# Performance work log

Measured on AMD Instinct MI355X. Metric: run time of the kernel, lower is better.

The kernel has to match this reference:

```python
import jax, jax.numpy as jnp
import numpy as np

D_IN, D_DICT, K, N = 768, 16384, 32, 8192


def setup_inputs() -> dict:
    key = jax.random.key(0)
    k1, k2, k3, k4, k5 = jax.random.split(key, 5)
    s_in = 1.0 / np.sqrt(D_IN)
    s_dict = 1.0 / np.sqrt(D_DICT)
    return {
        "x": jax.random.normal(k1, (N, D_IN), dtype=jnp.float32),
        # torch Linear: weight [out, in], bias [out]
        "W_enc": jax.random.uniform(k2, (D_DICT, D_IN), jnp.float32, -s_in, s_in),
        "b_enc": jax.random.uniform(k3, (D_DICT,), jnp.float32, -s_in, s_in),
        "W_dec": jax.random.uniform(k4, (D_IN, D_DICT), jnp.float32, -s_dict, s_dict),
        "b_dec": jax.random.uniform(k5, (D_IN,), jnp.float32, -s_dict, s_dict),
    }


def reference(x, W_enc, b_enc, W_dec, b_dec):
    # encode: z = x @ W_enc^T + b_enc  -> [N, d_dict]
    z = jnp.einsum("nd,kd->nk", x, W_enc) + b_enc
    # top-k mask along last dim (scatter 1.0 at top-k indices)
    _, idx = jax.lax.top_k(z, K)                      # idx: [N, K]
    rows = jnp.arange(z.shape[0])[:, None]            # [N, 1]
    mask = jnp.zeros_like(z).at[rows, idx].set(1.0)
    z_sparse = z * mask
    # decode: x_hat = z_sparse @ W_dec^T + b_dec -> [N, d_in]
    x_hat = jnp.einsum("nk,dk->nd", z_sparse, W_dec) + b_dec
    return (x_hat, z_sparse)
```

## Files before the change

### kernel.cpp

```cpp
#include <hip/hip_runtime.h>
#include <stdint.h>

#define D_IN   768
#define D_DICT 16384
#define NROWS  8192
#define TOPK   32
#define CAND_TARGET 40
#define CAND_MAX    80

typedef __attribute__((ext_vector_type(4))) float  f32x4;
typedef __attribute__((ext_vector_type(8))) short  s16x8;
typedef __attribute__((ext_vector_type(4))) unsigned short u16x4;

static __device__ __forceinline__ unsigned short f2bf(float f) {
    unsigned int u = __float_as_uint(f);
    unsigned int r = (u + 0x7FFFu + ((u >> 16) & 1u)) >> 16;
    return (unsigned short)r;
}

static __device__ __forceinline__ void gload_lds16(const void* g, void* l) {
    __builtin_amdgcn_global_load_lds(
        (const __attribute__((address_space(1))) unsigned int*)g,
        (__attribute__((address_space(3))) unsigned int*)l, 16, 0, 0);
}

__global__ __launch_bounds__(256) void cast_bf16(const float4* __restrict__ in,
                                                 u16x4* __restrict__ out, int n4) {
    int idx = blockIdx.x * 256 + threadIdx.x;
    if (idx >= n4) return;
    float4 v = in[idx];
    u16x4 o;
    o.x = f2bf(v.x); o.y = f2bf(v.y); o.z = f2bf(v.z); o.w = f2bf(v.w);
    out[idx] = o;
}

__global__ void transpose_wdec(const float* __restrict__ in, float* __restrict__ out) {
    __shared__ float t[32][33];
    int bx = blockIdx.x;
    int by = blockIdx.y;
    int tx = threadIdx.x;
    int ty = threadIdx.y;
#pragma unroll
    for (int i = 0; i < 4; ++i)
        t[ty + i * 8][tx] = in[(size_t)(by * 32 + ty + i * 8) * D_DICT + bx * 32 + tx];
    __syncthreads();
#pragma unroll
    for (int i = 0; i < 4; ++i)
        out[(size_t)(bx * 32 + ty + i * 8) * D_IN + by * 32 + tx] = t[tx][ty + i * 8];
}

__global__ __launch_bounds__(256) void gemm_enc(const unsigned short* __restrict__ Xb,
                                                const unsigned short* __restrict__ Wb,
                                                const float* __restrict__ bEnc,
                                                float* __restrict__ zbase) {
    __shared__ unsigned short As[128 * 64];
    __shared__ unsigned short Bs[128 * 64];
    const int tid    = threadIdx.x;
    const int waveId = tid >> 6;
    const int lane   = tid & 63;
    const int rowBase = blockIdx.y * 128;
    const int colBase = blockIdx.x * 128;
    const int wm = waveId >> 1, wn = waveId & 1;

    f32x4 acc[4][4] = {};

    const int m0 = wm * 64 + (lane & 15);
    const int n0 = wn * 64 + (lane & 15);
    const int kq = (lane >> 4) * 8;

    for (int k0 = 0; k0 < D_IN; k0 += 64) {
#pragma unroll
        for (int i = 0; i < 4; ++i) {
            int slot = i * 256 + tid;
            int r = slot >> 3, cc = (slot & 7) * 8;
            const unsigned short* ga = Xb + (size_t)(rowBase + r) * D_IN + k0 + cc;
            const unsigned short* gb = Wb + (size_t)(colBase + r) * D_IN + k0 + cc;
            unsigned short* la = As + (size_t)(i * 256 + waveId * 64) * 8;
            unsigned short* lb = Bs + (size_t)(i * 256 + waveId * 64) * 8;
            gload_lds16(ga, la);
            gload_lds16(gb, lb);
        }
        __syncthreads();
#pragma unroll
        for (int kk = 0; kk < 64; kk += 32) {
            s16x8 a[4], b[4];
#pragma unroll
            for (int t = 0; t < 4; ++t) {
                a[t] = *(const s16x8*)(As + (m0 + t * 16) * 64 + kk + kq);
                b[t] = *(const s16x8*)(Bs + (n0 + t * 16) * 64 + kk + kq);
            }
#pragma unroll
            for (int mi = 0; mi < 4; ++mi)
#pragma unroll
                for (int ni = 0; ni < 4; ++ni)
                    acc[mi][ni] = __builtin_amdgcn_mfma_f32_16x16x32_bf16(
                        a[mi], b[ni], acc[mi][ni], 0, 0, 0);
        }
        __syncthreads();
    }

    const int col0 = colBase + wn * 64 + (lane & 15);
    const int rq   = (lane >> 4) * 4;
#pragma unroll
    for (int ni = 0; ni < 4; ++ni) {
        int gc = col0 + ni * 16;
        float bias = bEnc[gc];
#pragma unroll
        for (int mi = 0; mi < 4; ++mi) {
            int gr0 = rowBase + wm * 64 + mi * 16 + rq;
#pragma unroll
            for (int rg = 0; rg < 4; ++rg) {
                float v = acc[mi][ni][rg] + bias;
                ((unsigned short*)(zbase + (size_t)(gr0 + rg) * D_DICT))[gc] = f2bf(v);
            }
        }
    }
}

__global__ __launch_bounds__(256) void rowpass(const float* __restrict__ x,
                                               const float* __restrict__ wEnc,
                                               const float* __restrict__ bEnc,
                                               const float* __restrict__ bDec,
                                               const float* __restrict__ wDecT,
                                               float* __restrict__ xhat,
                                               float* __restrict__ zsp) {
    const int row = blockIdx.x;
    const int tid = threadIdx.x;

    __shared__ unsigned short zrow[D_DICT];
    __shared__ int   hist[256];
    __shared__ float xs[D_IN];
    __shared__ int   cidx[CAND_MAX];
    __shared__ float zc[CAND_MAX];
    __shared__ int   selk[TOPK];
    __shared__ float selv[TOPK];
    __shared__ int   sh_nstrict, sh_ntie, sh_nsel, sh_cutHi, sh_cumAbove, sh_cut;

    hist[tid] = 0;
    if (tid == 0) { sh_nstrict = 0; sh_ntie = 0; sh_nsel = 0; }
    __syncthreads();

    const unsigned short* zr = (const unsigned short*)(zsp + (size_t)row * D_DICT);
#pragma unroll 2
    for (int i = 0; i < 8; ++i) {
        uint4 raw = ((const uint4*)zr)[i * 256 + tid];
        unsigned int w[4] = {raw.x, raw.y, raw.z, raw.w};
        int base = (i * 256 + tid) * 8;
#pragma unroll
        for (int q = 0; q < 4; ++q) {
#pragma unroll
            for (int h = 0; h < 2; ++h) {
                unsigned short u = (unsigned short)((w[q] >> (16 * h)) & 0xFFFFu);
                u = (u & 0x8000u) ? (unsigned short)(~u) : (unsigned short)(u | 0x8000u);
                zrow[base + q * 2 + h] = u;
                atomicAdd(&hist[u >> 8], 1);
            }
        }
    }
    for (int j = tid; j < D_IN; j += 256) xs[j] = x[(size_t)row * D_IN + j];
    __syncthreads();

    {
        float4 z4 = make_float4(0.f, 0.f, 0.f, 0.f);
        float4* zd = (float4*)(zsp + (size_t)row * D_DICT);
#pragma unroll 4
        for (int i = 0; i < 16; ++i) zd[i * 256 + tid] = z4;
    }

    if (tid == 0) {
        int cum = 0, b = 255;
        for (; b >= 0; --b) {
            int c = cum + hist[b];
            if (c >= CAND_TARGET) break;
            cum = c;
        }
        sh_cutHi = b; sh_cumAbove = cum;
    }
    __syncthreads();
    const int cutHi = sh_cutHi;
    hist[tid] = 0;
    __syncthreads();
    for (int i = 0; i < 64; ++i) {
        unsigned short u = zrow[i * 256 + tid];
        if ((u >> 8) == cutHi) atomicAdd(&hist[u & 255], 1);
    }
    __syncthreads();
    if (tid == 0) {
        int cum = sh_cumAbove, b = 255;
        for (; b >= 0; --b) {
            int c = cum + hist[b];
            if (c >= CAND_TARGET) break;
            cum = c;
        }
        sh_cut = (cutHi << 8) | b;
    }
    __syncthreads();
    const unsigned short cut = (unsigned short)sh_cut;

    for (int i = 0; i < 64; ++i) {
        int idx = i * 256 + tid;
        unsigned short u = zrow[idx];
        if (u > cut) {
            int p = atomicAdd(&sh_nstrict, 1);
            cidx[p] = idx;
        } else if (u == cut) {
            int t = atomicAdd(&sh_ntie, 1);
            if (t < CAND_TARGET) cidx[CAND_MAX - 1 - t] = idx;
        }
    }
    __syncthreads();
    const int nstrict = sh_nstrict;
    const int nt = min(sh_ntie, CAND_TARGET);
    int tmpv = 0;
    if (tid < nt) tmpv = cidx[CAND_MAX - 1 - tid];
    __syncthreads();
    if (tid < nt) cidx[nstrict + tid] = tmpv;
    __syncthreads();
    const int nc = nstrict + nt;

    const int wave = tid >> 6, lane = tid & 63;
    for (int c = wave; c < nc; c += 4) {
        int k = cidx[c];
        const float* w = wEnc + (size_t)k * D_IN;
        double acc = 0.0;
#pragma unroll
        for (int i = 0; i < D_IN / 64; ++i) {
            int j = i * 64 + lane;
            acc += (double)xs[j] * (double)w[j];
        }
#pragma unroll
        for (int off = 32; off > 0; off >>= 1) acc += __shfl_xor(acc, off, 64);
        if (lane == 0) zc[c] = (float)(acc + (double)bEnc[k]);
    }
    __syncthreads();

    if (tid < nc) {
        float v = zc[tid];
        int   k = cidx[tid];
        int r = 0;
        for (int j = 0; j < nc; ++j) {
            float vj = zc[j];
            if (vj > v || (vj == v && cidx[j] < k)) ++r;
        }
        if (r < TOPK) {
            int s = atomicAdd(&sh_nsel, 1);
            selk[s] = k; selv[s] = v;
            zsp[(size_t)row * D_DICT + k] = v;
        }
    }
    __syncthreads();

    for (int d = tid; d < D_IN; d += 256) {
        float acc = bDec[d];
#pragma unroll
        for (int j = 0; j < TOPK; ++j)
            acc += selv[j] * wDecT[(size_t)selk[j] * D_IN + d];
        xhat[(size_t)row * D_IN + d] = acc;
    }
}

extern "C" void kernel_launch(void* const* d_in, const int* in_sizes, int n_in,
                              void* d_out, int out_size, void* d_ws, size_t ws_size,
                              hipStream_t stream) {
    const float* x    = (const float*)d_in[0];
    const float* wEnc = (const float*)d_in[1];
    const float* bEnc = (const float*)d_in[2];
    const float* wDec = (const float*)d_in[3];
    const float* bDec = (const float*)d_in[4];

    float* xhat = (float*)d_out;
    float* zsp  = (float*)d_out + (size_t)NROWS * D_IN;

    char* ws = (char*)d_ws;
    unsigned short* Xb  = (unsigned short*)ws;
    unsigned short* Wb  = (unsigned short*)(ws + (size_t)NROWS * D_IN * 2);
    float*          WdT = (float*)(ws + (size_t)NROWS * D_IN * 2
                                      + (size_t)D_DICT * D_IN * 2);

    {
        int n4 = NROWS * D_IN / 4;
        cast_bf16<<<(n4 + 255) / 256, 256, 0, stream>>>((const float4*)x, (u16x4*)Xb, n4);
    }
    {
        int n4 = D_DICT * D_IN / 4;
        cast_bf16<<<(n4 + 255) / 256, 256, 0, stream>>>((const float4*)wEnc, (u16x4*)Wb, n4);
    }
    transpose_wdec<<<dim3(D_DICT / 32, D_IN / 32), dim3(32, 8), 0, stream>>>(wDec, WdT);
    gemm_enc<<<dim3(D_DICT / 128, NROWS / 128), 256, 0, stream>>>(Xb, Wb, bEnc, zsp);
    rowpass<<<NROWS, 256, 0, stream>>>(x, wEnc, bEnc, bDec, WdT, xhat, zsp);
}
```

Baseline: 1.397 ms.

## Restructure top-k selection into register-resident histogram pass and separate decode kernel

The encoder GEMM now writes the order-preserving mapped bf16 scores into a densely packed buffer that aliases the z_sparse output. A new selection kernel keeps each row's scores in registers instead of staging them in LDS. It builds per-wave histograms, first over a floored range with a fallback to the full range, and finds the threshold bins with wave prefix scans and ballots rather than a serial single-thread loop. Candidate rescoring now uses four threads per candidate instead of a whole wave. Zeroing and scattering z_sparse and the decode move to a separate kernel, which is needed because the packed scores overlap the output; this costs an extra launch and a small index/value round trip through the workspace.

After: 1.352 ms. -3.2%, faster.

```diff
diff --git a/kernel.cpp b/kernel.cpp
--- a/kernel.cpp
+++ b/kernel.cpp
@@ -16,6 +16,9 @@
     unsigned int u = __float_as_uint(f);
     unsigned int r = (u + 0x7FFFu + ((u >> 16) & 1u)) >> 16;
     return (unsigned short)r;
+}
+static __device__ __forceinline__ unsigned short bfmap(unsigned short u) {
+    return (u & 0x8000u) ? (unsigned short)(~u) : (unsigned short)(u | 0x8000u);
 }
 
 static __device__ __forceinline__ void gload_lds16(const void* g, void* l) {
@@ -36,10 +39,8 @@
 
 __global__ void transpose_wdec(const float* __restrict__ in, float* __restrict__ out) {
     __shared__ float t[32][33];
-    int bx = blockIdx.x;
-    int by = blockIdx.y;
-    int tx = threadIdx.x;
-    int ty = threadIdx.y;
+    int bx = blockIdx.x, by = blockIdx.y;
+    int tx = threadIdx.x, ty = threadIdx.y;
 #pragma unroll
     for (int i = 0; i < 4; ++i)
         t[ty + i * 8][tx] = in[(size_t)(by * 32 + ty + i * 8) * D_DICT + bx * 32 + tx];
@@ -52,7 +53,7 @@
 __global__ __launch_bounds__(256) void gemm_enc(const unsigned short* __restrict__ Xb,
                                                 const unsigned short* __restrict__ Wb,
                                                 const float* __restrict__ bEnc,
-                                                float* __restrict__ zbase) {
+                                                unsigned short* __restrict__ zhat) {
     __shared__ unsigned short As[128 * 64];
     __shared__ unsigned short Bs[128 * 64];
     const int tid    = threadIdx.x;
@@ -111,102 +112,153 @@
 #pragma unroll
             for (int rg = 0; rg < 4; ++rg) {
                 float v = acc[mi][ni][rg] + bias;
-                ((unsigned short*)(zbase + (size_t)(gr0 + rg) * D_DICT))[gc] = f2bf(v);
-            }
-        }
-    }
-}
-
-__global__ __launch_bounds__(256) void rowpass(const float* __restrict__ x,
-                                               const float* __restrict__ wEnc,
-                                               const float* __restrict__ bEnc,
-                                               const float* __restrict__ bDec,
-                                               const float* __restrict__ wDecT,
-                                               float* __restrict__ xhat,
-                                               float* __restrict__ zsp) {
+                zhat[(size_t)(gr0 + rg) * D_DICT + gc] = bfmap(f2bf(v));
+            }
+        }
+    }
+}
+
+__global__ __launch_bounds__(256) void sel_topk(const unsigned short* __restrict__ zhat,
+                                                const float* __restrict__ x,
+                                                const float* __restrict__ wEnc,
+                                                const float* __restrict__ bEnc,
+                                                int* __restrict__ SelK,
+                                                float* __restrict__ SelV) {
     const int row = blockIdx.x;
     const int tid = threadIdx.x;
-
-    __shared__ unsigned short zrow[D_DICT];
-    __shared__ int   hist[256];
+    const int waveId = tid >> 6;
+
+    __shared__ int   histc[4][256];
     __shared__ float xs[D_IN];
     __shared__ int   cidx[CAND_MAX];
     __shared__ float zc[CAND_MAX];
     __shared__ int   selk[TOPK];
     __shared__ float selv[TOPK];
-    __shared__ int   sh_nstrict, sh_ntie, sh_nsel, sh_cutHi, sh_cumAbove, sh_cut;
-
-    hist[tid] = 0;
+    __shared__ int   sh_bin, sh_cum, sh_bin2;
+    __shared__ int   sh_nstrict, sh_ntie, sh_nsel;
+
+    uint4 r[8];
+    const uint4* zr4 = (const uint4*)(zhat + (size_t)row * D_DICT);
+#pragma unroll
+    for (int i = 0; i < 8; ++i) r[i] = zr4[i * 256 + tid];
+    for (int j = tid; j < D_IN; j += 256) xs[j] = x[(size_t)row * D_IN + j];
     if (tid == 0) { sh_nstrict = 0; sh_ntie = 0; sh_nsel = 0; }
-    __syncthreads();
-
-    const unsigned short* zr = (const unsigned short*)(zsp + (size_t)row * D_DICT);
-#pragma unroll 2
+
+    unsigned int floorU = 0xBE80u;
+    int shift1 = 6;
+    const int T = CAND_TARGET;
+
+    for (int att = 0; att < 2; ++att) {
+        for (int b = tid; b < 1024; b += 256) ((int*)histc)[b] = 0;
+        if (tid == 0) sh_bin = -1;
+        __syncthreads();
+#pragma unroll
+        for (int i = 0; i < 8; ++i) {
+            unsigned int w[4] = {r[i].x, r[i].y, r[i].z, r[i].w};
+#pragma unroll
+            for (int q = 0; q < 4; ++q)
+#pragma unroll
+                for (int h = 0; h < 2; ++h) {
+                    unsigned int u = (w[q] >> (16 * h)) & 0xFFFFu;
+                    if (u >= floorU) {
+                        int bin = (int)((u - floorU) >> shift1);
+                        if (bin > 255) bin = 255;
+                        atomicAdd(&histc[waveId][bin], 1);
+                    }
+                }
+        }
+        __syncthreads();
+        if (tid < 256) histc[0][tid] += histc[1][tid] + histc[2][tid] + histc[3][tid];
+        __syncthreads();
+        if (tid < 64) {
+            int l = tid;
+            int b0 = 255 - l * 4;
+            int s0 = histc[0][b0], s1 = histc[0][b0 - 1],
+                s2 = histc[0][b0 - 2], s3 = histc[0][b0 - 3];
+            int local = s0 + s1 + s2 + s3;
+            int pref = local;
+#pragma unroll
+            for (int off = 1; off < 64; off <<= 1) {
+                int n = __shfl_up(pref, off, 64);
+                if (l >= off) pref += n;
+            }
+            unsigned long long m = __ballot(pref >= T);
+            if (m) {
+                int first = (int)__ffsll(m) - 1;
+                if (l == first) {
+                    int cum = pref - local;
+                    int b, c;
+                    if      (cum + s0 >= T)           { b = b0;     c = cum; }
+                    else if (cum + s0 + s1 >= T)      { b = b0 - 1; c = cum + s0; }
+                    else if (cum + s0 + s1 + s2 >= T) { b = b0 - 2; c = cum + s0 + s1; }
+                    else                              { b = b0 - 3; c = cum + s0 + s1 + s2; }
+                    sh_bin = b; sh_cum = c;
+                }
+            }
+        }
+        __syncthreads();
+        if (sh_bin >= 0) break;
+        floorU = 0u; shift1 = 8;
+    }
+    const int b1 = sh_bin;
+    const int cumAbove = sh_cum;
+    const int s2 = shift1 - 6;
+
+    for (int b = tid; b < 1024; b += 256) ((int*)histc)[b] = 0;
+    __syncthreads();
+#pragma unroll
     for (int i = 0; i < 8; ++i) {
-        uint4 raw = ((const uint4*)zr)[i * 256 + tid];
-        unsigned int w[4] = {raw.x, raw.y, raw.z, raw.w};
-        int base = (i * 256 + tid) * 8;
-#pragma unroll
-        for (int q = 0; q < 4; ++q) {
+        unsigned int w[4] = {r[i].x, r[i].y, r[i].z, r[i].w};
+#pragma unroll
+        for (int q = 0; q < 4; ++q)
 #pragma unroll
             for (int h = 0; h < 2; ++h) {
-                unsigned short u = (unsigned short)((w[q] >> (16 * h)) & 0xFFFFu);
-                u = (u & 0x8000u) ? (unsigned short)(~u) : (unsigned short)(u | 0x8000u);
-                zrow[base + q * 2 + h] = u;
-                atomicAdd(&hist[u >> 8], 1);
-            }
-        }
-    }
-    for (int j = tid; j < D_IN; j += 256) xs[j] = x[(size_t)row * D_IN + j];
-    __syncthreads();
-
-    {
-        float4 z4 = make_float4(0.f, 0.f, 0.f, 0.f);
-        float4* zd = (float4*)(zsp + (size_t)row * D_DICT);
-#pragma unroll 4
-        for (int i = 0; i < 16; ++i) zd[i * 256 + tid] = z4;
-    }
-
-    if (tid == 0) {
-        int cum = 0, b = 255;
-        for (; b >= 0; --b) {
-            int c = cum + hist[b];
-            if (c >= CAND_TARGET) break;
-            cum = c;
-        }
-        sh_cutHi = b; sh_cumAbove = cum;
-    }
-    __syncthreads();
-    const int cutHi = sh_cutHi;
-    hist[tid] = 0;
-    __syncthreads();
-    for (int i = 0; i < 64; ++i) {
-        unsigned short u = zrow[i * 256 + tid];
-        if ((u >> 8) == cutHi) atomicAdd(&hist[u & 255], 1);
-    }
-    __syncthreads();
-    if (tid == 0) {
-        int cum = sh_cumAbove, b = 255;
-        for (; b >= 0; --b) {
-            int c = cum + hist[b];
-            if (c >= CAND_TARGET) break;
-            cum = c;
-        }
-        sh_cut = (cutHi << 8) | b;
-    }
-    __syncthreads();
-    const unsigned short cut = (unsigned short)sh_cut;
-
-    for (int i = 0; i < 64; ++i) {
-        int idx = i * 256 + tid;
-        unsigned short u = zrow[idx];
-        if (u > cut) {
-            int p = atomicAdd(&sh_nstrict, 1);
-            cidx[p] = idx;
-        } else if (u == cut) {
-            int t = atomicAdd(&sh_ntie, 1);
-            if (t < CAND_TARGET) cidx[CAND_MAX - 1 - t] = idx;
-        }
+                unsigned int u = (w[q] >> (16 * h)) & 0xFFFFu;
+                if (u >= floorU) {
+                    int bin = (int)((u - floorU) >> shift1);
+                    if (bin > 255) bin = 255;
+                    if (bin == b1) {
+                        int bin2 = (int)(((u - floorU) >> s2) & 63u);
+                        atomicAdd(&histc[waveId][bin2], 1);
+                    }
+                }
+            }
+    }
+    __syncthreads();
+    if (tid < 64) {
+        int l = tid;
+        int bb = 63 - l;
+        int local = histc[0][bb] + histc[1][bb] + histc[2][bb] + histc[3][bb];
+        int pref = local;
+#pragma unroll
+        for (int off = 1; off < 64; off <<= 1) {
+            int n = __shfl_up(pref, off, 64);
+            if (l >= off) pref += n;
+        }
+        unsigned long long m = __ballot(cumAbove + pref >= T);
+        int first = (int)__ffsll(m) - 1;
+        if (l == first) sh_bin2 = bb;
+    }
+    __syncthreads();
+    const unsigned int tieLo  = floorU + ((unsigned)b1 << shift1) + ((unsigned)sh_bin2 << s2);
+    const unsigned int tieTop = tieLo + (1u << s2) - 1u;
+
+#pragma unroll
+    for (int i = 0; i < 8; ++i) {
+        unsigned int w[4] = {r[i].x, r[i].y, r[i].z, r[i].w};
+#pragma unroll
+        for (int q = 0; q < 4; ++q)
+#pragma unroll
+            for (int h = 0; h < 2; ++h) {
+                unsigned int u = (w[q] >> (16 * h)) & 0xFFFFu;
+                if (u > tieTop) {
+                    int p = atomicAdd(&sh_nstrict, 1);
+                    cidx[p] = (i * 256 + tid) * 8 + q * 2 + h;
+                } else if (u >= tieLo) {
+                    int t = atomicAdd(&sh_ntie, 1);
+                    if (t < CAND_TARGET) cidx[CAND_MAX - 1 - t] = (i * 256 + tid) * 8 + q * 2 + h;
+                }
+            }
     }
     __syncthreads();
     const int nstrict = sh_nstrict;
@@ -218,43 +270,71 @@
     __syncthreads();
     const int nc = nstrict + nt;
 
-    const int wave = tid >> 6, lane = tid & 63;
-    for (int c = wave; c < nc; c += 4) {
-        int k = cidx[c];
-        const float* w = wEnc + (size_t)k * D_IN;
+    const int sub = tid & 3;
+    const int cq  = tid >> 2;
+    for (int c0 = 0; c0 < nc; c0 += 64) {
+        int c = c0 + cq;
         double acc = 0.0;
-#pragma unroll
-        for (int i = 0; i < D_IN / 64; ++i) {
-            int j = i * 64 + lane;
-            acc += (double)xs[j] * (double)w[j];
-        }
-#pragma unroll
-        for (int off = 32; off > 0; off >>= 1) acc += __shfl_xor(acc, off, 64);
-        if (lane == 0) zc[c] = (float)(acc + (double)bEnc[k]);
+        int k = 0;
+        if (c < nc) {
+            k = cidx[c];
+            const float* w  = wEnc + (size_t)k * D_IN + sub * 192;
+            const float* xp = xs + sub * 192;
+#pragma unroll 8
+            for (int j = 0; j < 192; ++j) acc += (double)xp[j] * (double)w[j];
+        }
+        acc += __shfl_xor(acc, 1, 64);
+        acc += __shfl_xor(acc, 2, 64);
+        if (c < nc && sub == 0) zc[c] = (float)(acc + (double)bEnc[k]);
     }
     __syncthreads();
 
     if (tid < nc) {
         float v = zc[tid];
         int   k = cidx[tid];
-        int r = 0;
+        int rk = 0;
         for (int j = 0; j < nc; ++j) {
             float vj = zc[j];
-            if (vj > v || (vj == v && cidx[j] < k)) ++r;
-        }
-        if (r < TOPK) {
+            if (vj > v || (vj == v && cidx[j] < k)) ++rk;
+        }
+        if (rk < TOPK) {
             int s = atomicAdd(&sh_nsel, 1);
             selk[s] = k; selv[s] = v;
-            zsp[(size_t)row * D_DICT + k] = v;
-        }
-    }
-    __syncthreads();
+        }
+    }
+    __syncthreads();
+    if (tid < TOPK) {
+        SelK[(size_t)row * TOPK + tid] = selk[tid];
+        SelV[(size_t)row * TOPK + tid] = selv[tid];
+    }
+}
+
+__global__ __launch_bounds__(256) void zdec(const int* __restrict__ SelK,
+                                            const float* __restrict__ SelV,
+                                            const float* __restrict__ wDecT,
+                                            const float* __restrict__ bDec,
+                                            float* __restrict__ zsp,
+                                            float* __restrict__ xhat) {
+    const int row = blockIdx.x;
+    const int tid = threadIdx.x;
+    __shared__ int   sk[TOPK];
+    __shared__ float sv[TOPK];
+    if (tid < TOPK) {
+        sk[tid] = SelK[(size_t)row * TOPK + tid];
+        sv[tid] = SelV[(size_t)row * TOPK + tid];
+    }
+    float4 z4 = make_float4(0.f, 0.f, 0.f, 0.f);
+    float4* zd = (float4*)(zsp + (size_t)row * D_DICT);
+#pragma unroll
+    for (int i = 0; i < 16; ++i) zd[i * 256 + tid] = z4;
+    __syncthreads();
+    if (tid < TOPK) zsp[(size_t)row * D_DICT + sk[tid]] = sv[tid];
 
     for (int d = tid; d < D_IN; d += 256) {
         float acc = bDec[d];
 #pragma unroll
         for (int j = 0; j < TOPK; ++j)
-            acc += selv[j] * wDecT[(size_t)selk[j] * D_IN + d];
+            acc += sv[j] * wDecT[(size_t)sk[j] * D_IN + d];
         xhat[(size_t)row * D_IN + d] = acc;
     }
 }
@@ -270,12 +350,15 @@
 
     float* xhat = (float*)d_out;
     float* zsp  = (float*)d_out + (size_t)NROWS * D_IN;
+    unsigned short* zhat = (unsigned short*)zsp;
 
     char* ws = (char*)d_ws;
     unsigned short* Xb  = (unsigned short*)ws;
     unsigned short* Wb  = (unsigned short*)(ws + (size_t)NROWS * D_IN * 2);
     float*          WdT = (float*)(ws + (size_t)NROWS * D_IN * 2
                                       + (size_t)D_DICT * D_IN * 2);
+    int*   SelK = (int*)(ws + 88080384);
+    float* SelV = (float*)(ws + 88080384 + (size_t)NROWS * TOPK * 4);
 
     {
         int n4 = NROWS * D_IN / 4;
@@ -286,6 +369,7 @@
         cast_bf16<<<(n4 + 255) / 256, 256, 0, stream>>>((const float4*)wEnc, (u16x4*)Wb, n4);
     }
     transpose_wdec<<<dim3(D_DICT / 32, D_IN / 32), dim3(32, 8), 0, stream>>>(wDec, WdT);
-    gemm_enc<<<dim3(D_DICT / 128, NROWS / 128), 256, 0, stream>>>(Xb, Wb, bEnc, zsp);
-    rowpass<<<NROWS, 256, 0, stream>>>(x, wEnc, bEnc, bDec, WdT, xhat, zsp);
-}
+    gemm_enc<<<dim3(D_DICT / 128, NROWS / 128), 256, 0, stream>>>(Xb, Wb, bEnc, zhat);
+    sel_topk<<<NROWS, 256, 0, stream>>>(zhat, x, wEnc, bEnc, SelK, SelV);
+    zdec<<<NROWS, 256, 0, stream>>>(SelK, SelV, WdT, bDec, zsp, xhat);
+}
```
